# Kernel tuning notes

Measured on AMD Instinct MI355X. Metric: run time of the kernel, lower is better.

The kernel has to match this reference:

```python
import jax, jax.numpy as jnp
import numpy as np

NUM_HEADS = 8
OUT_DIM = 16
IN_DIM = 128
N_NODES = 50000
N_EDGES = 1600000


def setup_inputs() -> dict:
    key = jax.random.key(0)
    ks = jax.random.split(key, 10)
    s = 1.0 / np.sqrt(IN_DIM)
    return {
        "h": jax.random.normal(ks[0], (N_NODES, IN_DIM), dtype=jnp.float32),
        "Qw": jax.random.normal(ks[1], (NUM_HEADS * OUT_DIM, IN_DIM), dtype=jnp.float32) * s,
        "Qb": jax.random.normal(ks[2], (NUM_HEADS * OUT_DIM,), dtype=jnp.float32) * 0.01,
        "Kw": jax.random.normal(ks[3], (NUM_HEADS * OUT_DIM, IN_DIM), dtype=jnp.float32) * s,
        "Kb": jax.random.normal(ks[4], (NUM_HEADS * OUT_DIM,), dtype=jnp.float32) * 0.01,
        "Vw": jax.random.normal(ks[5], (NUM_HEADS * OUT_DIM, IN_DIM), dtype=jnp.float32) * s,
        "Vb": jax.random.normal(ks[6], (NUM_HEADS * OUT_DIM,), dtype=jnp.float32) * 0.01,
        "src": jax.random.randint(ks[7], (N_EDGES,), 0, N_NODES, dtype=jnp.int64 if jax.config.jax_enable_x64 else jnp.int32).astype(jnp.int32),
        "dst": jax.random.randint(ks[8], (N_EDGES,), 0, N_NODES, dtype=jnp.int64 if jax.config.jax_enable_x64 else jnp.int32).astype(jnp.int32),
    }


def reference(h, Qw, Qb, Kw, Kb, Vw, Vb, src, dst):
    N = h.shape[0]
    H, D = NUM_HEADS, OUT_DIM
    # Q/K/V projections (torch Linear: x @ W.T + b), viewed as [N, H, D]
    Q = (h @ Qw.T + Qb).reshape(N, H, D)
    K = (h @ Kw.T + Kb).reshape(N, H, D)
    V = (h @ Vw.T + Vb).reshape(N, H, D)

    # dgl.add_self_loop: append (i, i) edges for every node
    loop = jnp.arange(N, dtype=src.dtype)
    s = jnp.concatenate([src, loop])
    d = jnp.concatenate([dst, loop])

    # src_dot_dst quirk: matmul(K_src [H,D], Q_dst^T [D,H]).sum(-1)
    # => score[e, h] = K_src[e, h] . (sum over heads of Q_dst[e])
    Qsum = Q.sum(axis=1)  # [N, D]
    score = jnp.einsum("ehd,ed->eh", K[s], Qsum[d])  # [E', H]
    score = jnp.exp(jnp.clip(score / np.float32(np.sqrt(D)), -5.0, 5.0))

    # scatter-sum of weighted V and scores to destination nodes
    wV = jax.ops.segment_sum(V[s] * score[:, :, None], d, num_segments=N)  # [N, H, D]
    z = jax.ops.segment_sum(score, d, num_segments=N)  # [N, H]

    head_out = wV / z[:, :, None]  # self-loops guarantee z > 0
    return head_out.mean(axis=1)  # [N, D]
```

## Files before the change

### kernel.cpp

```cpp
#include <hip/hip_runtime.h>
#include <hip/hip_fp16.h>
#include <math.h>

#define NNODES 50000
#define IND    128
#define NH     8
#define OD     16
#define NEDGE  1600000
#define NOUT   272
#define NBUCK  391
#define BCAP   4608
#define P1B    196
#define CB     3125
#define PB2    782

typedef _Float16 half8 __attribute__((ext_vector_type(8)));
typedef _Float16 h2t   __attribute__((ext_vector_type(2)));
typedef float    floatx4 __attribute__((ext_vector_type(4)));

static __device__ __forceinline__ h2t u2h(unsigned int u) {
    union { unsigned int u; h2t h; } x; x.u = u; return x.h;
}
static __device__ __forceinline__ float qdot(uint4 k, uint4 q, float p) {
    p = __builtin_amdgcn_fdot2(u2h(k.x), u2h(q.x), p, false);
    p = __builtin_amdgcn_fdot2(u2h(k.y), u2h(q.y), p, false);
    p = __builtin_amdgcn_fdot2(u2h(k.z), u2h(q.z), p, false);
    p = __builtin_amdgcn_fdot2(u2h(k.w), u2h(q.w), p, false);
    return p;
}
static __device__ __forceinline__ void vacc8(uint4 vA, uint4 vB, h2t sc2, float* acc) {
    unsigned lo, hi;
    lo = __builtin_amdgcn_perm(vB.x, vA.x, 0x05040100u);
    hi = __builtin_amdgcn_perm(vB.x, vA.x, 0x07060302u);
    acc[0] = __builtin_amdgcn_fdot2(u2h(lo), sc2, acc[0], false);
    acc[1] = __builtin_amdgcn_fdot2(u2h(hi), sc2, acc[1], false);
    lo = __builtin_amdgcn_perm(vB.y, vA.y, 0x05040100u);
    hi = __builtin_amdgcn_perm(vB.y, vA.y, 0x07060302u);
    acc[2] = __builtin_amdgcn_fdot2(u2h(lo), sc2, acc[2], false);
    acc[3] = __builtin_amdgcn_fdot2(u2h(hi), sc2, acc[3], false);
    lo = __builtin_amdgcn_perm(vB.z, vA.z, 0x05040100u);
    hi = __builtin_amdgcn_perm(vB.z, vA.z, 0x07060302u);
    acc[4] = __builtin_amdgcn_fdot2(u2h(lo), sc2, acc[4], false);
    acc[5] = __builtin_amdgcn_fdot2(u2h(hi), sc2, acc[5], false);
    lo = __builtin_amdgcn_perm(vB.w, vA.w, 0x05040100u);
    hi = __builtin_amdgcn_perm(vB.w, vA.w, 0x07060302u);
    acc[6] = __builtin_amdgcn_fdot2(u2h(lo), sc2, acc[6], false);
    acc[7] = __builtin_amdgcn_fdot2(u2h(hi), sc2, acc[7], false);
}

__global__ __launch_bounds__(256) void k1_conv(
    const float* __restrict__ hmat,
    const float* __restrict__ Qw, const float* __restrict__ Qb,
    const float* __restrict__ Kw, const float* __restrict__ Kb,
    const float* __restrict__ Vw, const float* __restrict__ Vb,
    _Float16* __restrict__ h16, _Float16* __restrict__ W16,
    float* __restrict__ b_all, int* __restrict__ cursor)
{
    const int bid = blockIdx.x;
    const int t   = threadIdx.x;

    if (bid < CB) {
        const size_t i = (size_t)bid * 256 + t;
        const float4* hp = (const float4*)hmat;
        float4 x = hp[i * 2];
        float4 y = hp[i * 2 + 1];
        half8 o;
        o[0] = (_Float16)x.x; o[1] = (_Float16)x.y;
        o[2] = (_Float16)x.z; o[3] = (_Float16)x.w;
        o[4] = (_Float16)y.x; o[5] = (_Float16)y.y;
        o[6] = (_Float16)y.z; o[7] = (_Float16)y.w;
        *(half8*)(h16 + i * 8) = o;
        return;
    }
    for (int i = t; i < NOUT * IND; i += 256) {
        int r = i >> 7, c = i & 127;
        float v;
        if (r < 128)       v = Kw[i];
        else if (r < 256)  v = Vw[i - 128 * IND];
        else {
            v = 0.f;
#pragma unroll
            for (int hh = 0; hh < NH; hh++) v += Qw[((hh << 4) + (r - 256)) * IND + c];
        }
        W16[i] = (_Float16)v;
    }
    for (int i = t; i < NOUT; i += 256) {
        float v;
        if (i < 128)      v = Kb[i];
        else if (i < 256) v = Vb[i - 128];
        else {
            v = 0.f;
#pragma unroll
            for (int hh = 0; hh < NH; hh++) v += Qb[(hh << 4) + (i - 256)];
        }
        b_all[i] = v;
    }
    for (int i = t; i < NBUCK; i += 256) cursor[i] = i * BCAP;
}

__global__ __launch_bounds__(256) void k2_scatter_proj(
    const int* __restrict__ src, const int* __restrict__ dst,
    int* __restrict__ cursor, unsigned int* __restrict__ ebuck,
    const _Float16* __restrict__ h16, const _Float16* __restrict__ W16,
    const float* __restrict__ b_all,
    __half* __restrict__ KVbuf, _Float16* __restrict__ Qs16)
{
    const int t = threadIdx.x;

    if (blockIdx.x < P1B) {
        __shared__ int bcnt[NBUCK];
        __shared__ int baseg[NBUCK];
        for (int i = t; i < NBUCK; i += 256) bcnt[i] = 0;
        __syncthreads();

        const int e0 = blockIdx.x * 8192;
        const int nq = (min(8192, NEDGE - e0)) >> 2;
        const int4* s4 = (const int4*)(src + e0);
        const int4* d4 = (const int4*)(dst + e0);

        uint4 ev4[8];
        unsigned int rkp[16];
#pragma unroll
        for (int j = 0; j < 8; j++) {
            int qi = j * 256 + t;
            if (qi < nq) {
                int4 ss = s4[qi];
                int4 dd = d4[qi];
                unsigned int v0 = (((unsigned)dd.x >> 7) << 23) | ((unsigned)ss.x << 7) | ((unsigned)dd.x & 127u);
                unsigned int v1 = (((unsigned)dd.y >> 7) << 23) | ((unsigned)ss.y << 7) | ((unsigned)dd.y & 127u);
                unsigned int v2 = (((unsigned)dd.z >> 7) << 23) | ((unsigned)ss.z << 7) | ((unsigned)dd.z & 127u);
                unsigned int v3 = (((unsigned)dd.w >> 7) << 23) | ((unsigned)ss.w << 7) | ((unsigned)dd.w & 127u);
                ev4[j] = make_uint4(v0, v1, v2, v3);
                unsigned r0 = atomicAdd(&bcnt[v0 >> 23], 1);
                unsigned r1 = atomicAdd(&bcnt[v1 >> 23], 1);
                unsigned r2 = atomicAdd(&bcnt[v2 >> 23], 1);
                unsigned r3 = atomicAdd(&bcnt[v3 >> 23], 1);
                rkp[2 * j]     = r0 | (r1 << 16);
                rkp[2 * j + 1] = r2 | (r3 << 16);
            }
        }
        __syncthreads();
        for (int i = t; i < NBUCK; i += 256)
            if (bcnt[i]) baseg[i] = atomicAdd(&cursor[i], bcnt[i]);
        __syncthreads();
#pragma unroll
        for (int j = 0; j < 8; j++) {
            int qi = j * 256 + t;
            if (qi < nq) {
                uint4 v = ev4[j];
                unsigned p0 = rkp[2 * j], p1 = rkp[2 * j + 1];
                ebuck[baseg[v.x >> 23] + (p0 & 0xFFFFu)] = v.x;
                ebuck[baseg[v.y >> 23] + (p0 >> 16)]     = v.y;
                ebuck[baseg[v.z >> 23] + (p1 & 0xFFFFu)] = v.z;
                ebuck[baseg[v.w >> 23] + (p1 >> 16)]     = v.w;
            }
        }
        return;
    }

    const int pbid = blockIdx.x - P1B;
    const int wave = t >> 6;
    const int l    = t & 63;
    const int cl   = l & 15;
    const int quad = l >> 4;
    const int m0   = pbid * 64 + wave * 16;

    const _Float16* ab = h16 + (size_t)(m0 + cl) * IND + quad * 8;
    half8 afrag[4];
#pragma unroll
    for (int ks = 0; ks < 4; ks++) afrag[ks] = *(const half8*)(ab + ks * 32);

    const int rowbase = m0 + quad * 4;

#pragma unroll 4
    for (int ti = 0; ti < 17; ti++) {
        const _Float16* wb = W16 + (size_t)(ti * 16 + cl) * IND + quad * 8;
        floatx4 acc = {0.f, 0.f, 0.f, 0.f};
#pragma unroll
        for (int ks = 0; ks < 4; ks++)
            acc = __builtin_amdgcn_mfma_f32_16x16x32_f16(
                afrag[ks], *(const half8*)(wb + ks * 32), acc, 0, 0, 0);

        const float bias = b_all[ti * 16 + cl];
        if (ti < 16) {
            const int col = ti * 16 + cl;
#pragma unroll
            for (int r = 0; r < 4; r++) {
                int node = rowbase + r;
                if (node < NNODES)
                    KVbuf[(size_t)node * 256 + col] = __float2half_rn(acc[r] + bias);
            }
        } else {
#pragma unroll
            for (int r = 0; r < 4; r++) {
                int node = rowbase + r;
                if (node < NNODES)
                    Qs16[(size_t)node * OD + cl] = (_Float16)(acc[r] + bias);
            }
        }
    }
}

__global__ __launch_bounds__(256) void k3_group(
    const unsigned int* __restrict__ ebuck, const int* __restrict__ cursor,
    int* __restrict__ offs, int* __restrict__ count,
    unsigned short* __restrict__ eidx16)
{
    __shared__ int cnt[128];
    __shared__ int base128[128];
    const int b = blockIdx.x;
    const int t = threadIdx.x;
    const int start = b * BCAP;
    const int end   = cursor[b];

    if (t < 128) cnt[t] = 0;
    __syncthreads();

    int rk[18];
#pragma unroll
    for (int j = 0; j < 18; j++) {
        int i = start + j * 256 + t;
        if (i < end) rk[j] = atomicAdd(&cnt[ebuck[i] & 127], 1);
    }
    __syncthreads();

    int c = 0, v = 0;
    if (t < 128) { c = cnt[t]; v = c; }
    for (int ofs = 1; ofs < 128; ofs <<= 1) {
        int x = (t >= ofs && t < 128) ? base128[0] : 0;
        (void)x;
        __syncthreads();
        if (t < 128) base128[t] = v;
        __syncthreads();
        if (t >= ofs && t < 128) v += base128[t - ofs];
    }
    __syncthreads();
    if (t < 128) {
        int excl = v - c;
        base128[t] = excl;
        int node = (b << 7) + t;
        if (node < NNODES) { offs[node] = start + excl; count[node] = c; }
    }
    __syncthreads();

#pragma unroll
    for (int j = 0; j < 18; j++) {
        int i = start + j * 256 + t;
        if (i < end) {
            unsigned int e = ebuck[i];
            eidx16[start + base128[e & 127] + rk[j]] =
                (unsigned short)((e >> 7) & 0xFFFFu);
        }
    }
}

__global__ __launch_bounds__(256) void k4_gather(
    const uint4* __restrict__ KV4, const uint4* __restrict__ Qs16u4,
    const int* __restrict__ offs, const int* __restrict__ count,
    const unsigned short* __restrict__ eidx16,
    float* __restrict__ out)
{
    const int n = blockIdx.x * 4 + (threadIdx.x >> 6);
    const int l = threadIdx.x & 63;
    if (n >= NNODES) return;

    const int lh = l & 15;
    const int eg = l >> 4;
    const int la = 2 * eg, lb = 2 * eg + 1;

    const uint4 qh = Qs16u4[n * 2 + (lh & 1)];

    const int off   = offs[n];
    const int total = count[n] + 1;

    float acc[8] = {0.f, 0.f, 0.f, 0.f, 0.f, 0.f, 0.f, 0.f};
    float zacc = 0.f;

    for (int base = 0; base < total; base += 64) {
        const int gi = base + l;
        int id = n;
        if (gi > 0) id = (gi < total) ? (int)eidx16[off + gi - 1] : 0;
        const int steps = min(64, total - base);

        int sA = __shfl(id, la, 64), sB = __shfl(id, lb, 64);
        uint4 kA0 = KV4[(size_t)sA * 32 + lh];
        uint4 vA0 = KV4[(size_t)sA * 32 + 16 + lh];
        uint4 kB0 = KV4[(size_t)sB * 32 + lh];
        uint4 vB0 = KV4[(size_t)sB * 32 + 16 + lh];
        int n1a = 8 + la, n1b = 8 + lb;
        int sA1 = __shfl(id, (n1a < 64) ? n1a : 0, 64);
        int sB1 = __shfl(id, (n1b < 64) ? n1b : 0, 64);
        uint4 kA1 = KV4[(size_t)sA1 * 32 + lh];
        uint4 vA1 = KV4[(size_t)sA1 * 32 + 16 + lh];
        uint4 kB1 = KV4[(size_t)sB1 * 32 + lh];
        uint4 vB1 = KV4[(size_t)sB1 * 32 + 16 + lh];

        for (int j = 0; j < steps; j += 8) {
            uint4 kA2, vA2, kB2, vB2;
            if (j + 16 < steps) {
                int n2a = j + 16 + la, n2b = j + 16 + lb;
                int sA2 = __shfl(id, (n2a < 64) ? n2a : 0, 64);
                int sB2 = __shfl(id, (n2b < 64) ? n2b : 0, 64);
                kA2 = KV4[(size_t)sA2 * 32 + lh];
                vA2 = KV4[(size_t)sA2 * 32 + 16 + lh];
                kB2 = KV4[(size_t)sB2 * 32 + lh];
                vB2 = KV4[(size_t)sB2 * 32 + 16 + lh];
            }
            float pA = qdot(kA0, qh, 0.f);
            float pB = qdot(kB0, qh, 0.f);
            pA += __shfl_xor(pA, 1, 64);
            pB += __shfl_xor(pB, 1, 64);
            float scA = __expf(fminf(5.f, fmaxf(-5.f, pA * 0.25f)));
            float scB = __expf(fminf(5.f, fmaxf(-5.f, pB * 0.25f)));
            if (j + la >= steps) scA = 0.f;
            if (j + lb >= steps) scB = 0.f;
            zacc += scA + scB;
            h2t sc2; sc2.x = (_Float16)scA; sc2.y = (_Float16)scB;
            vacc8(vA0, vB0, sc2, acc);
            kA0 = kA1; vA0 = vA1; kB0 = kB1; vB0 = vB1;
            kA1 = kA2; vA1 = vA2; kB1 = kB2; vB1 = vB2;
        }
    }

#pragma unroll
    for (int i = 0; i < 8; i++) {
        acc[i] += __shfl_xor(acc[i], 16, 64);
        acc[i] += __shfl_xor(acc[i], 32, 64);
    }
    zacc += __shfl_xor(zacc, 16, 64);
    zacc += __shfl_xor(zacc, 32, 64);

    const float inv = 1.f / zacc;
    float r[8];
#pragma unroll
    for (int i = 0; i < 8; i++) r[i] = acc[i] * inv;
#pragma unroll
    for (int i = 0; i < 8; i++) {
        r[i] += __shfl_xor(r[i], 2, 64);
        r[i] += __shfl_xor(r[i], 4, 64);
        r[i] += __shfl_xor(r[i], 8, 64);
    }
    if (l < 2) {
        float4* op = (float4*)(out + (size_t)n * OD + l * 8);
        op[0] = make_float4(r[0] * 0.125f, r[1] * 0.125f, r[2] * 0.125f, r[3] * 0.125f);
        op[1] = make_float4(r[4] * 0.125f, r[5] * 0.125f, r[6] * 0.125f, r[7] * 0.125f);
    }
}

extern "C" void kernel_launch(void* const* d_in, const int* in_sizes, int n_in,
                              void* d_out, int out_size, void* d_ws, size_t ws_size,
                              hipStream_t stream)
{
    const float* h  = (const float*)d_in[0];
    const float* Qw = (const float*)d_in[1];
    const float* Qb = (const float*)d_in[2];
    const float* Kw = (const float*)d_in[3];
    const float* Kb = (const float*)d_in[4];
    const float* Vw = (const float*)d_in[5];
    const float* Vb = (const float*)d_in[6];
    const int*   src = (const int*)d_in[7];
    const int*   dst = (const int*)d_in[8];

    char* ws = (char*)d_ws;
    _Float16* h16   = (_Float16*)ws;                   ws += (size_t)50048 * IND * 2;
    _Float16* W16   = (_Float16*)ws;                   ws += (size_t)NOUT * IND * 2;
    float*    b_all = (float*)ws;                      ws += 288 * 4;
    __half*   KVbuf = (__half*)ws;                     ws += (size_t)NNODES * 256 * 2;
    _Float16* Qs16  = (_Float16*)ws;                   ws += (size_t)NNODES * OD * 2;
    int*      offs   = (int*)ws;                       ws += (size_t)NNODES * 4;
    int*      count  = (int*)ws;                       ws += (size_t)NNODES * 4;
    int*      cursor = (int*)ws;                       ws += 1024 * 4;
    unsigned int*   ebuck  = (unsigned int*)ws;        ws += (size_t)NBUCK * BCAP * 4;
    unsigned short* eidx16 = (unsigned short*)ws;      ws += (size_t)NBUCK * BCAP * 2;

    k1_conv<<<CB + 1, 256, 0, stream>>>(
        h, Qw, Qb, Kw, Kb, Vw, Vb, h16, W16, b_all, cursor);

    k2_scatter_proj<<<P1B + PB2, 256, 0, stream>>>(
        src, dst, cursor, ebuck, h16, W16, b_all, KVbuf, Qs16);

    k3_group<<<NBUCK, 256, 0, stream>>>(ebuck, cursor, offs, count, eidx16);

    k4_gather<<<(NNODES + 3) / 4, 256, 0, stream>>>(
        (const uint4*)KVbuf, (const uint4*)Qs16, offs, count, eidx16, (float*)d_out);
}
```

Measured before the change: 279.9 us.

## Fuse h fp16 conversion into projection and merge projection with bucket grouping

Removes the separate pass that converted h to fp16; the projection blocks now load fp32 h and convert it in registers. The pipeline is regrouped so edge bucketing runs alongside the weight conversion, and the projection runs in the same launch as per-bucket grouping. This drops one kernel launch and the h16 write/read round trip, at the cost of a memset to reset bucket counters. The prefix scan is also rewritten in a simpler shared-memory form.

```diff
diff --git a/kernel.cpp b/kernel.cpp
--- a/kernel.cpp
+++ b/kernel.cpp
@@ -11,7 +11,6 @@
 #define NBUCK  391
 #define BCAP   4608
 #define P1B    196
-#define CB     3125
 #define PB2    782
 
 typedef _Float16 half8 __attribute__((ext_vector_type(8)));
@@ -48,62 +47,13 @@
     acc[7] = __builtin_amdgcn_fdot2(u2h(hi), sc2, acc[7], false);
 }
 
-__global__ __launch_bounds__(256) void k1_conv(
-    const float* __restrict__ hmat,
+__global__ __launch_bounds__(256) void ka_scatter_w16(
+    const int* __restrict__ src, const int* __restrict__ dst,
+    int* __restrict__ bcount, unsigned int* __restrict__ ebuck,
     const float* __restrict__ Qw, const float* __restrict__ Qb,
     const float* __restrict__ Kw, const float* __restrict__ Kb,
     const float* __restrict__ Vw, const float* __restrict__ Vb,
-    _Float16* __restrict__ h16, _Float16* __restrict__ W16,
-    float* __restrict__ b_all, int* __restrict__ cursor)
-{
-    const int bid = blockIdx.x;
-    const int t   = threadIdx.x;
-
-    if (bid < CB) {
-        const size_t i = (size_t)bid * 256 + t;
-        const float4* hp = (const float4*)hmat;
-        float4 x = hp[i * 2];
-        float4 y = hp[i * 2 + 1];
-        half8 o;
-        o[0] = (_Float16)x.x; o[1] = (_Float16)x.y;
-        o[2] = (_Float16)x.z; o[3] = (_Float16)x.w;
-        o[4] = (_Float16)y.x; o[5] = (_Float16)y.y;
-        o[6] = (_Float16)y.z; o[7] = (_Float16)y.w;
-        *(half8*)(h16 + i * 8) = o;
-        return;
-    }
-    for (int i = t; i < NOUT * IND; i += 256) {
-        int r = i >> 7, c = i & 127;
-        float v;
-        if (r < 128)       v = Kw[i];
-        else if (r < 256)  v = Vw[i - 128 * IND];
-        else {
-            v = 0.f;
-#pragma unroll
-            for (int hh = 0; hh < NH; hh++) v += Qw[((hh << 4) + (r - 256)) * IND + c];
-        }
-        W16[i] = (_Float16)v;
-    }
-    for (int i = t; i < NOUT; i += 256) {
-        float v;
-        if (i < 128)      v = Kb[i];
-        else if (i < 256) v = Vb[i - 128];
-        else {
-            v = 0.f;
-#pragma unroll
-            for (int hh = 0; hh < NH; hh++) v += Qb[(hh << 4) + (i - 256)];
-        }
-        b_all[i] = v;
-    }
-    for (int i = t; i < NBUCK; i += 256) cursor[i] = i * BCAP;
-}
-
-__global__ __launch_bounds__(256) void k2_scatter_proj(
-    const int* __restrict__ src, const int* __restrict__ dst,
-    int* __restrict__ cursor, unsigned int* __restrict__ ebuck,
-    const _Float16* __restrict__ h16, const _Float16* __restrict__ W16,
-    const float* __restrict__ b_all,
-    __half* __restrict__ KVbuf, _Float16* __restrict__ Qs16)
+    _Float16* __restrict__ W16, float* __restrict__ b_all)
 {
     const int t = threadIdx.x;
 
@@ -141,7 +91,7 @@
         }
         __syncthreads();
         for (int i = t; i < NBUCK; i += 256)
-            if (bcnt[i]) baseg[i] = atomicAdd(&cursor[i], bcnt[i]);
+            if (bcnt[i]) baseg[i] = i * BCAP + atomicAdd(&bcount[i], bcnt[i]);
         __syncthreads();
 #pragma unroll
         for (int j = 0; j < 8; j++) {
@@ -158,60 +108,101 @@
         return;
     }
 
-    const int pbid = blockIdx.x - P1B;
-    const int wave = t >> 6;
-    const int l    = t & 63;
-    const int cl   = l & 15;
-    const int quad = l >> 4;
-    const int m0   = pbid * 64 + wave * 16;
-
-    const _Float16* ab = h16 + (size_t)(m0 + cl) * IND + quad * 8;
-    half8 afrag[4];
-#pragma unroll
-    for (int ks = 0; ks < 4; ks++) afrag[ks] = *(const half8*)(ab + ks * 32);
-
-    const int rowbase = m0 + quad * 4;
-
-#pragma unroll 4
-    for (int ti = 0; ti < 17; ti++) {
-        const _Float16* wb = W16 + (size_t)(ti * 16 + cl) * IND + quad * 8;
-        floatx4 acc = {0.f, 0.f, 0.f, 0.f};
-#pragma unroll
-        for (int ks = 0; ks < 4; ks++)
-            acc = __builtin_amdgcn_mfma_f32_16x16x32_f16(
-                afrag[ks], *(const half8*)(wb + ks * 32), acc, 0, 0, 0);
-
-        const float bias = b_all[ti * 16 + cl];
-        if (ti < 16) {
-            const int col = ti * 16 + cl;
-#pragma unroll
-            for (int r = 0; r < 4; r++) {
-                int node = rowbase + r;
-                if (node < NNODES)
-                    KVbuf[(size_t)node * 256 + col] = __float2half_rn(acc[r] + bias);
-            }
-        } else {
-#pragma unroll
-            for (int r = 0; r < 4; r++) {
-                int node = rowbase + r;
-                if (node < NNODES)
-                    Qs16[(size_t)node * OD + cl] = (_Float16)(acc[r] + bias);
-            }
-        }
-    }
-}
-
-__global__ __launch_bounds__(256) void k3_group(
-    const unsigned int* __restrict__ ebuck, const int* __restrict__ cursor,
+    for (int i = t; i < NOUT * IND; i += 256) {
+        int r = i >> 7, c = i & 127;
+        float v;
+        if (r < 128)       v = Kw[i];
+        else if (r < 256)  v = Vw[i - 128 * IND];
+        else {
+            v = 0.f;
+#pragma unroll
+            for (int hh = 0; hh < NH; hh++) v += Qw[((hh << 4) + (r - 256)) * IND + c];
+        }
+        W16[i] = (_Float16)v;
+    }
+    for (int i = t; i < NOUT; i += 256) {
+        float v;
+        if (i < 128)      v = Kb[i];
+        else if (i < 256) v = Vb[i - 128];
+        else {
+            v = 0.f;
+#pragma unroll
+            for (int hh = 0; hh < NH; hh++) v += Qb[(hh << 4) + (i - 256)];
+        }
+        b_all[i] = v;
+    }
+}
+
+__global__ __launch_bounds__(256) void kb_proj_group(
+    const float* __restrict__ hmat,
+    const _Float16* __restrict__ W16, const float* __restrict__ b_all,
+    __half* __restrict__ KVbuf, _Float16* __restrict__ Qs16,
+    const unsigned int* __restrict__ ebuck, const int* __restrict__ bcount,
     int* __restrict__ offs, int* __restrict__ count,
     unsigned short* __restrict__ eidx16)
 {
+    const int t = threadIdx.x;
+
+    if (blockIdx.x < PB2) {
+        const int wave = t >> 6;
+        const int l    = t & 63;
+        const int cl   = l & 15;
+        const int quad = l >> 4;
+        const int m0   = blockIdx.x * 64 + wave * 16;
+
+        const int arow = min(m0 + cl, NNODES - 1);
+        const float* ab = hmat + (size_t)arow * IND + quad * 8;
+        half8 afrag[4];
+#pragma unroll
+        for (int ks = 0; ks < 4; ks++) {
+            float4 x = *(const float4*)(ab + ks * 32);
+            float4 y = *(const float4*)(ab + ks * 32 + 4);
+            half8 o;
+            o[0] = (_Float16)x.x; o[1] = (_Float16)x.y;
+            o[2] = (_Float16)x.z; o[3] = (_Float16)x.w;
+            o[4] = (_Float16)y.x; o[5] = (_Float16)y.y;
+            o[6] = (_Float16)y.z; o[7] = (_Float16)y.w;
+            afrag[ks] = o;
+        }
+
+        const int rowbase = m0 + quad * 4;
+
+#pragma unroll 4
+        for (int ti = 0; ti < 17; ti++) {
+            const _Float16* wb = W16 + (size_t)(ti * 16 + cl) * IND + quad * 8;
+            floatx4 acc = {0.f, 0.f, 0.f, 0.f};
+#pragma unroll
+            for (int ks = 0; ks < 4; ks++)
+                acc = __builtin_amdgcn_mfma_f32_16x16x32_f16(
+                    afrag[ks], *(const half8*)(wb + ks * 32), acc, 0, 0, 0);
+
+            const float bias = b_all[ti * 16 + cl];
+            if (ti < 16) {
+                const int col = ti * 16 + cl;
+#pragma unroll
+                for (int r = 0; r < 4; r++) {
+                    int node = rowbase + r;
+                    if (node < NNODES)
+                        KVbuf[(size_t)node * 256 + col] = __float2half_rn(acc[r] + bias);
+                }
+            } else {
+#pragma unroll
+                for (int r = 0; r < 4; r++) {
+                    int node = rowbase + r;
+                    if (node < NNODES)
+                        Qs16[(size_t)node * OD + cl] = (_Float16)(acc[r] + bias);
+                }
+            }
+        }
+        return;
+    }
+
     __shared__ int cnt[128];
+    __shared__ int sd[128];
     __shared__ int base128[128];
-    const int b = blockIdx.x;
-    const int t = threadIdx.x;
+    const int b = blockIdx.x - PB2;
     const int start = b * BCAP;
-    const int end   = cursor[b];
+    const int end   = start + bcount[b];
 
     if (t < 128) cnt[t] = 0;
     __syncthreads();
@@ -224,22 +215,20 @@
     }
     __syncthreads();
 
-    int c = 0, v = 0;
-    if (t < 128) { c = cnt[t]; v = c; }
+    if (t < 128) sd[t] = cnt[t];
+    __syncthreads();
     for (int ofs = 1; ofs < 128; ofs <<= 1) {
-        int x = (t >= ofs && t < 128) ? base128[0] : 0;
-        (void)x;
-        __syncthreads();
-        if (t < 128) base128[t] = v;
-        __syncthreads();
-        if (t >= ofs && t < 128) v += base128[t - ofs];
-    }
-    __syncthreads();
+        int x = 0;
+        if (t < 128 && t >= ofs) x = sd[t - ofs];
+        __syncthreads();
+        if (t < 128) sd[t] += x;
+        __syncthreads();
+    }
     if (t < 128) {
-        int excl = v - c;
+        int excl = sd[t] - cnt[t];
         base128[t] = excl;
         int node = (b << 7) + t;
-        if (node < NNODES) { offs[node] = start + excl; count[node] = c; }
+        if (node < NNODES) { offs[node] = start + excl; count[node] = cnt[t]; }
     }
     __syncthreads();
 
@@ -254,7 +243,7 @@
     }
 }
 
-__global__ __launch_bounds__(256) void k4_gather(
+__global__ __launch_bounds__(256) void kc_gather(
     const uint4* __restrict__ KV4, const uint4* __restrict__ Qs16u4,
     const int* __restrict__ offs, const int* __restrict__ count,
     const unsigned short* __restrict__ eidx16,
@@ -362,25 +351,24 @@
     const int*   dst = (const int*)d_in[8];
 
     char* ws = (char*)d_ws;
-    _Float16* h16   = (_Float16*)ws;                   ws += (size_t)50048 * IND * 2;
     _Float16* W16   = (_Float16*)ws;                   ws += (size_t)NOUT * IND * 2;
     float*    b_all = (float*)ws;                      ws += 288 * 4;
     __half*   KVbuf = (__half*)ws;                     ws += (size_t)NNODES * 256 * 2;
     _Float16* Qs16  = (_Float16*)ws;                   ws += (size_t)NNODES * OD * 2;
     int*      offs   = (int*)ws;                       ws += (size_t)NNODES * 4;
     int*      count  = (int*)ws;                       ws += (size_t)NNODES * 4;
-    int*      cursor = (int*)ws;                       ws += 1024 * 4;
+    int*      bcount = (int*)ws;                       ws += 1024 * 4;
     unsigned int*   ebuck  = (unsigned int*)ws;        ws += (size_t)NBUCK * BCAP * 4;
     unsigned short* eidx16 = (unsigned short*)ws;      ws += (size_t)NBUCK * BCAP * 2;
 
-    k1_conv<<<CB + 1, 256, 0, stream>>>(
-        h, Qw, Qb, Kw, Kb, Vw, Vb, h16, W16, b_all, cursor);
-
-    k2_scatter_proj<<<P1B + PB2, 256, 0, stream>>>(
-        src, dst, cursor, ebuck, h16, W16, b_all, KVbuf, Qs16);
-
-    k3_group<<<NBUCK, 256, 0, stream>>>(ebuck, cursor, offs, count, eidx16);
-
-    k4_gather<<<(NNODES + 3) / 4, 256, 0, stream>>>(
+    hipMemsetAsync(bcount, 0, 1024 * 4, stream);
+
+    ka_scatter_w16<<<P1B + 1, 256, 0, stream>>>(
+        src, dst, bcount, ebuck, Qw, Qb, Kw, Kb, Vw, Vb, W16, b_all);
+
+    kb_proj_group<<<PB2 + NBUCK, 256, 0, stream>>>(
+        h, W16, b_all, KVbuf, Qs16, ebuck, bcount, offs, count, eidx16);
+
+    kc_gather<<<(NNODES + 3) / 4, 256, 0, stream>>>(
         (const uint4*)KVbuf, (const uint4*)Qs16, offs, count, eidx16, (float*)d_out);
 }
```

After: 270.2 us. 1.04x faster.
